# Optimization experiments

Hardware: AMD Instinct MI355X
Metric: run time of the kernel (lower is better)

Reference implementation:

```python
import jax, jax.numpy as jnp
import numpy as np

EPS = 1e-15


def setup_inputs() -> dict:
    key = jax.random.key(0)
    ks = jax.random.split(key, 10)
    F, B, L = 10, 16384, 20          # num_field, batch, hist_len
    V, D = 1000000, 16               # sparse_feature_number, sparse_feature_dim
    FEAT, E, S, G, T = 160, 8, 64, 3, 32  # feature_size, expert_num, expert_size, gate_num, tower_size
    return {
        "ids": jax.random.randint(ks[0], (F, B, L), 0, V, dtype=jnp.int64),
        "emb_table": jax.random.uniform(ks[1], (V, D), jnp.float32, -1.0, 1.0),
        "expert_w": jax.random.normal(ks[2], (E, FEAT, S), jnp.float32) * 0.05,
        "expert_b": jnp.full((E, S), 0.1, jnp.float32),
        "gate_w": jax.random.normal(ks[3], (G, FEAT, E), jnp.float32) * 0.05,
        "gate_b": jnp.full((G, E), 0.1, jnp.float32),
        "tower_w": jax.random.normal(ks[4], (G, S, T), jnp.float32) * 0.05,
        "tower_b": jnp.full((G, T), 0.1, jnp.float32),
        "out_w": jax.random.normal(ks[5], (G, T, 2), jnp.float32) * 0.05,
        "out_b": jnp.full((G, 2), 0.1, jnp.float32),
    }


def reference(ids, emb_table, expert_w, expert_b, gate_w, gate_b,
              tower_w, tower_b, out_w, out_b):
    # Embedding lookup + sum over history: [F,B,L,D] -> [F,B,D]
    field_emb = emb_table[ids].sum(axis=2)
    B = field_emb.shape[1]
    # concat per-field embeddings along feature axis: [B, F*D]
    x = jnp.transpose(field_emb, (1, 0, 2)).reshape(B, -1)
    # all experts as one batched GEMM: [B,E,S]
    experts = jax.nn.relu(jnp.einsum('bf,efs->bes', x, expert_w) + expert_b)
    # gate softmax over experts: [B,G,E]
    gates = jax.nn.softmax(jnp.einsum('bf,gfe->bge', x, gate_w) + gate_b, axis=-1)
    # gate-weighted expert mixture: [B,G,S]
    mix = jnp.einsum('bge,bes->bgs', gates, experts)
    # towers: [B,G,T] -> logits [B,G,2]
    tow = jax.nn.relu(jnp.einsum('bgs,gst->bgt', mix, tower_w) + tower_b)
    logits = jnp.einsum('bgt,gto->bgo', tow, out_w) + out_b
    probs = jnp.clip(jax.nn.softmax(logits, axis=-1), EPS, 1.0 - EPS)  # [B,3,2]
    ctr, cvr, imp = probs[:, 0], probs[:, 1], probs[:, 2]
    ctr1 = ctr[:, 1:2]
    cvr1 = cvr[:, 1:2]
    ctcvr1 = ctr1 * cvr1
    ctcvr = jnp.concatenate([1.0 - ctcvr1, ctcvr1], axis=1)
    imp1 = imp[:, 1:2]
    # out_list packed along last axis: ctr(2), ctr1(1), cvr(2), cvr1(1), ctcvr(2), ctcvr1(1), imp1(1) -> [B,10]
    return jnp.concatenate([ctr, ctr1, cvr, cvr1, ctcvr, ctcvr1, imp1], axis=1)
```

## Files before the change

kernel.cpp:

```cpp
#include <hip/hip_runtime.h>
#include <hip/hip_bf16.h>
#include <cstdint>
#include <cstddef>

#define NFIELD 10
#define BATCH  16384
#define NIDS   20
#define DEMB   16
#define NFEAT  160
#define NEXP   8
#define NS     64
#define NG     3
#define NT     32

#define BP_OFF_B  0
#define BM_OFF_B  (BP_OFF_B + 174080)
#define BT_OFF_B  (BM_OFF_B + 2176)
#define TB2_OFF_B (BT_OFF_B + 12288)
#define OWF_OFF_B (TB2_OFF_B + 384)
#define OBF_OFF_B (OWF_OFF_B + 768)

typedef short bfrag __attribute__((ext_vector_type(8)));
typedef float f32x4 __attribute__((ext_vector_type(4)));

__device__ __forceinline__ float bflo(uint32_t u) {
    union { uint32_t u; float f; } c; c.u = u << 16; return c.f;
}
__device__ __forceinline__ float bfhi(uint32_t u) {
    union { uint32_t u; float f; } c; c.u = u & 0xffff0000u; return c.f;
}
__device__ __forceinline__ float bf1(uint16_t v) {
    union { uint32_t u; float f; } c; c.u = ((uint32_t)v) << 16; return c.f;
}
__device__ __forceinline__ uint16_t f2bf(float f) {
    union { float f; uint32_t u; } c; c.f = f;
    uint32_t r = c.u + 0x7fffu + ((c.u >> 16) & 1u);
    return (uint16_t)(r >> 16);
}
__device__ __forceinline__ float ldw(const void* p, int i, bool bf) {
    return bf ? bf1(((const uint16_t*)p)[i]) : ((const float*)p)[i];
}
__device__ __forceinline__ uint16_t ldb16(const void* p, int i, bool bf) {
    return bf ? ((const uint16_t*)p)[i] : f2bf(((const float*)p)[i]);
}
__device__ __forceinline__ int sniff_bf(const uint32_t* emb_w) {
    int n_bf = 0;
    #pragma unroll
    for (int t = 0; t < 16; ++t) {
        uint32_t wv = emb_w[(size_t)t * 500000];
        uint32_t v = (wv >> 8) & 0x7Fu;
        n_bf += (v >= 0x3Bu && v <= 0x3Fu);
    }
    return n_bf >= 8;
}

__global__ __launch_bounds__(256) void pack_weights(
    const uint32_t* __restrict__ emb_w,
    const void* __restrict__ ew, const void* __restrict__ eb,
    const void* __restrict__ gw, const void* __restrict__ gb,
    const void* __restrict__ tw, const void* __restrict__ tb,
    const void* __restrict__ ow, const void* __restrict__ ob,
    uint16_t* __restrict__ bp, float* __restrict__ bm,
    uint16_t* __restrict__ bt, float* __restrict__ tb2,
    float* __restrict__ owf, float* __restrict__ obf)
{
    __shared__ int sbf;
    if (threadIdx.x == 0) sbf = sniff_bf(emb_w);
    __syncthreads();
    const bool bf = sbf != 0;

    int i = blockIdx.x * 256 + threadIdx.x;
    if (i < 10880) {
        int nt = i / 320, rem = i % 320;
        int ks = rem / 64, l = rem % 64;
        int n  = nt * 16 + (l & 15);
        int kb = ks * 32 + ((l >> 4) * 8);
        uint16_t v[8];
        #pragma unroll
        for (int j = 0; j < 8; ++j) {
            int k = kb + j;
            uint16_t x;
            if (n < 512)      x = ldb16(ew, (n >> 6) * 10240 + k * 64 + (n & 63), bf);
            else if (n < 536) x = ldb16(gw, ((n - 512) >> 3) * 1280 + k * 8 + ((n - 512) & 7), bf);
            else              x = 0;
            v[j] = x;
        }
        uint4 o;
        o.x = (uint32_t)v[0] | ((uint32_t)v[1] << 16);
        o.y = (uint32_t)v[2] | ((uint32_t)v[3] << 16);
        o.z = (uint32_t)v[4] | ((uint32_t)v[5] << 16);
        o.w = (uint32_t)v[6] | ((uint32_t)v[7] << 16);
        ((uint4*)bp)[i] = o;
    } else if (i < 11648) {
        int it = i - 10880;
        int g = it / 256, rem = it % 256;
        int ntile = rem / 128, ks = (rem / 64) & 1, l = rem % 64;
        int t  = ntile * 16 + (l & 15);
        int sb = ks * 32 + ((l >> 4) * 8);
        uint16_t v[8];
        #pragma unroll
        for (int j = 0; j < 8; ++j)
            v[j] = ldb16(tw, g * 2048 + (sb + j) * 32 + t, bf);
        uint4 o;
        o.x = (uint32_t)v[0] | ((uint32_t)v[1] << 16);
        o.y = (uint32_t)v[2] | ((uint32_t)v[3] << 16);
        o.z = (uint32_t)v[4] | ((uint32_t)v[5] << 16);
        o.w = (uint32_t)v[6] | ((uint32_t)v[7] << 16);
        ((uint4*)bt)[it] = o;
    } else if (i < 12192) {
        int n = i - 11648;
        bm[n] = (n < 512) ? ldw(eb, n, bf) : (n < 536 ? ldw(gb, n - 512, bf) : 0.0f);
    } else if (i < 12288) {
        int n = i - 12192; tb2[n] = ldw(tb, n, bf);
    } else if (i < 12480) {
        int n = i - 12288; owf[n] = ldw(ow, n, bf);
    } else if (i < 12486) {
        int n = i - 12480; obf[n] = ldw(ob, n, bf);
    }
}

__global__ __launch_bounds__(320, 3) void moe_fused(
    const void* __restrict__ ids_raw,
    const void* __restrict__ emb_raw,
    const uint16_t* __restrict__ bp,
    const float*    __restrict__ bm,
    const uint16_t* __restrict__ btw,
    const float*    __restrict__ btb,
    const float*    __restrict__ owf,
    const float*    __restrict__ obf,
    void* __restrict__ out)
{
    __shared__ uint16_t exp_lds[32][520];
    __shared__ float    gate_lds[32][33];
    __shared__ uint16_t mix_lds[32][200];
    __shared__ int      sflags;

    float* tow  = (float*)&exp_lds[0][0];
    float* prob = &gate_lds[0][0];

    const int tid = threadIdx.x;
    const int w = tid >> 6, l = tid & 63;
    const int lm = l & 15, q = l >> 4;
    const int b0 = blockIdx.x * 32;
    const int mrow = (w & 1) * 16;
    const int nhalf = w >> 1;

    if (tid == 0) {
        int n_hi = 0;
        #pragma unroll
        for (int t = 0; t < 16; ++t) {
            size_t p = (size_t)t * 100000;
            n_hi += (((const uint32_t*)ids_raw)[2 * p + 1] != 0);
        }
        sflags = ((n_hi < 2) ? 1 : 0) | (sniff_bf((const uint32_t*)emb_raw) ? 2 : 0);
    }
    __syncthreads();
    const bool i64 = (sflags & 1) != 0;
    const bool bfe = (sflags & 2) != 0;

    uint16_t* xs = &exp_lds[0][0];
    for (int p = tid; p < 32 * NFIELD; p += 320) {
        int f = p >> 5, s = p & 31;
        int idv[NIDS];
        if (i64) {
            const int4* p4 = (const int4*)((const long long*)ids_raw +
                                           ((size_t)f * BATCH + (b0 + s)) * NIDS);
            #pragma unroll
            for (int j = 0; j < NIDS / 2; ++j) {
                int4 t4 = p4[j];
                idv[2 * j + 0] = t4.x;
                idv[2 * j + 1] = t4.z;
            }
        } else {
            const int4* p4 = (const int4*)((const int*)ids_raw +
                                           ((size_t)f * BATCH + (b0 + s)) * NIDS);
            #pragma unroll
            for (int j = 0; j < NIDS / 4; ++j) {
                int4 t4 = p4[j];
                idv[4 * j + 0] = t4.x; idv[4 * j + 1] = t4.y;
                idv[4 * j + 2] = t4.z; idv[4 * j + 3] = t4.w;
            }
        }

        float acc[16];
        #pragma unroll
        for (int d = 0; d < 16; ++d) acc[d] = 0.0f;

        if (bfe) {
            #pragma unroll 5
            for (int ll = 0; ll < NIDS; ++ll) {
                const uint4* row = (const uint4*)((const uint16_t*)emb_raw +
                                                  (size_t)idv[ll] * DEMB);
                uint4 r0 = row[0];
                uint4 r1 = row[1];
                acc[0]  += bflo(r0.x); acc[1]  += bfhi(r0.x);
                acc[2]  += bflo(r0.y); acc[3]  += bfhi(r0.y);
                acc[4]  += bflo(r0.z); acc[5]  += bfhi(r0.z);
                acc[6]  += bflo(r0.w); acc[7]  += bfhi(r0.w);
                acc[8]  += bflo(r1.x); acc[9]  += bfhi(r1.x);
                acc[10] += bflo(r1.y); acc[11] += bfhi(r1.y);
                acc[12] += bflo(r1.z); acc[13] += bfhi(r1.z);
                acc[14] += bflo(r1.w); acc[15] += bfhi(r1.w);
            }
        } else {
            #pragma unroll 5
            for (int ll = 0; ll < NIDS; ++ll) {
                const float4* row = (const float4*)((const float*)emb_raw +
                                                    (size_t)idv[ll] * DEMB);
                float4 r0 = row[0], r1 = row[1], r2 = row[2], r3 = row[3];
                acc[0]  += r0.x; acc[1]  += r0.y; acc[2]  += r0.z; acc[3]  += r0.w;
                acc[4]  += r1.x; acc[5]  += r1.y; acc[6]  += r1.z; acc[7]  += r1.w;
                acc[8]  += r2.x; acc[9]  += r2.y; acc[10] += r2.z; acc[11] += r2.w;
                acc[12] += r3.x; acc[13] += r3.y; acc[14] += r3.z; acc[15] += r3.w;
            }
        }

        uint32_t pk[8];
        #pragma unroll
        for (int j = 0; j < 8; ++j)
            pk[j] = (uint32_t)f2bf(acc[2 * j]) | ((uint32_t)f2bf(acc[2 * j + 1]) << 16);
        uint4* dst = (uint4*)(xs + (size_t)s * 168 + f * DEMB);
        dst[0] = make_uint4(pk[0], pk[1], pk[2], pk[3]);
        dst[1] = make_uint4(pk[4], pk[5], pk[6], pk[7]);
    }
    __syncthreads();

    bfrag a[5];
    if (w < 4) {
        #pragma unroll
        for (int ks = 0; ks < 5; ++ks)
            a[ks] = *(const bfrag*)(xs + (size_t)(mrow + lm) * 168 + ks * 32 + q * 8);
    }
    __syncthreads();

    if (w < 4) {
        const int nt0 = nhalf * 17;
        for (int it = 0; it < 17; ++it) {
            int nt = nt0 + it;
            f32x4 acc = {0.0f, 0.0f, 0.0f, 0.0f};
            const bfrag* bpp = (const bfrag*)bp + (size_t)(nt * 5) * 64 + l;
            #pragma unroll
            for (int ks = 0; ks < 5; ++ks) {
                bfrag b = bpp[ks * 64];
                acc = __builtin_amdgcn_mfma_f32_16x16x32_bf16(a[ks], b, acc, 0, 0, 0);
            }
            int col = nt * 16 + lm;
            float bias = bm[col];
            if (col < 512) {
                #pragma unroll
                for (int r = 0; r < 4; ++r)
                    exp_lds[mrow + q * 4 + r][col] = f2bf(fmaxf(acc[r] + bias, 0.0f));
            } else {
                #pragma unroll
                for (int r = 0; r < 4; ++r)
                    gate_lds[mrow + q * 4 + r][col - 512] = acc[r] + bias;
            }
        }
    }
    __syncthreads();

    const int sm = tid >> 3, j = tid & 7;

    if (tid < 256 && j < 3) {
        float* gl = &gate_lds[sm][j * 8];
        float m = gl[0];
        #pragma unroll
        for (int e = 1; e < 8; ++e) m = fmaxf(m, gl[e]);
        float ex[8], s = 0.0f;
        #pragma unroll
        for (int e = 0; e < 8; ++e) { ex[e] = __expf(gl[e] - m); s += ex[e]; }
        float inv = 1.0f / s;
        #pragma unroll
        for (int e = 0; e < 8; ++e) gl[e] = ex[e] * inv;
    }
    __syncthreads();

    if (tid < 256) {
        for (int g = 0; g < NG; ++g) {
            float m8[8];
            #pragma unroll
            for (int i = 0; i < 8; ++i) m8[i] = 0.0f;
            #pragma unroll
            for (int e = 0; e < NEXP; ++e) {
                float gv = gate_lds[sm][g * 8 + e];
                uint4 u = *(const uint4*)&exp_lds[sm][e * 64 + j * 8];
                m8[0] = fmaf(gv, bflo(u.x), m8[0]); m8[1] = fmaf(gv, bfhi(u.x), m8[1]);
                m8[2] = fmaf(gv, bflo(u.y), m8[2]); m8[3] = fmaf(gv, bfhi(u.y), m8[3]);
                m8[4] = fmaf(gv, bflo(u.z), m8[4]); m8[5] = fmaf(gv, bfhi(u.z), m8[5]);
                m8[6] = fmaf(gv, bflo(u.w), m8[6]); m8[7] = fmaf(gv, bfhi(u.w), m8[7]);
            }
            uint4 o;
            o.x = (uint32_t)f2bf(m8[0]) | ((uint32_t)f2bf(m8[1]) << 16);
            o.y = (uint32_t)f2bf(m8[2]) | ((uint32_t)f2bf(m8[3]) << 16);
            o.z = (uint32_t)f2bf(m8[4]) | ((uint32_t)f2bf(m8[5]) << 16);
            o.w = (uint32_t)f2bf(m8[6]) | ((uint32_t)f2bf(m8[7]) << 16);
            *(uint4*)&mix_lds[sm][g * 64 + j * 8] = o;
        }
    }
    __syncthreads();

    for (int u = w; u < 12; u += 5) {
        int g = u >> 2, mt = (u >> 1) & 1, ntile = u & 1;
        f32x4 acc = {0.0f, 0.0f, 0.0f, 0.0f};
        #pragma unroll
        for (int ks = 0; ks < 2; ++ks) {
            bfrag av = *(const bfrag*)&mix_lds[mt * 16 + lm][g * 64 + ks * 32 + q * 8];
            bfrag bv = *(const bfrag*)(btw + (size_t)((((g * 2 + ntile) * 2 + ks) * 64 + l)) * 8);
            acc = __builtin_amdgcn_mfma_f32_16x16x32_bf16(av, bv, acc, 0, 0, 0);
        }
        int t = ntile * 16 + lm;
        float bias = btb[g * 32 + t];
        #pragma unroll
        for (int r = 0; r < 4; ++r)
            tow[(mt * 16 + q * 4 + r) * 100 + g * 32 + t] = fmaxf(acc[r] + bias, 0.0f);
    }
    __syncthreads();

    if (tid < 256 && j < 3) {
        int g = j;
        float l0 = obf[2 * g], l1 = obf[2 * g + 1];
        #pragma unroll 8
        for (int t = 0; t < NT; ++t) {
            float tv = tow[sm * 100 + g * 32 + t];
            l0 = fmaf(tv, owf[g * 64 + 2 * t], l0);
            l1 = fmaf(tv, owf[g * 64 + 2 * t + 1], l1);
        }
        float m  = fmaxf(l0, l1);
        float e0 = __expf(l0 - m);
        float e1 = __expf(l1 - m);
        float inv = 1.0f / (e0 + e1);
        float p0 = fminf(fmaxf(e0 * inv, 1e-15f), 1.0f);
        float p1 = fminf(fmaxf(e1 * inv, 1e-15f), 1.0f);
        prob[sm * 6 + 2 * g + 0] = p0;
        prob[sm * 6 + 2 * g + 1] = p1;
    }
    __syncthreads();

    if (tid < 256) {
        float ctr0 = prob[sm * 6 + 0], ctr1 = prob[sm * 6 + 1];
        float cvr0 = prob[sm * 6 + 2], cvr1 = prob[sm * 6 + 3];
        float imp1 = prob[sm * 6 + 5];
        float ctcvr1 = ctr1 * cvr1;
        for (int o = j; o < 10; o += 8) {
            float v;
            switch (o) {
                case 0: v = ctr0; break;
                case 1: v = ctr1; break;
                case 2: v = ctr1; break;
                case 3: v = cvr0; break;
                case 4: v = cvr1; break;
                case 5: v = cvr1; break;
                case 6: v = 1.0f - ctcvr1; break;
                case 7: v = ctcvr1; break;
                case 8: v = ctcvr1; break;
                default: v = imp1; break;
            }
            if (bfe) ((uint16_t*)out)[(size_t)(b0 + sm) * 10 + o] = f2bf(v);
            else     ((float*)out)[(size_t)(b0 + sm) * 10 + o]    = v;
        }
    }
}

extern "C" void kernel_launch(void* const* d_in, const int* in_sizes, int n_in,
                              void* d_out, int out_size, void* d_ws, size_t ws_size,
                              hipStream_t stream) {
    const void* ids = d_in[0];
    const void* emb = d_in[1];

    char* ws = (char*)d_ws;
    uint16_t* bpk = (uint16_t*)(ws + BP_OFF_B);
    float*    bm  = (float*)(ws + BM_OFF_B);
    uint16_t* btw = (uint16_t*)(ws + BT_OFF_B);
    float*    tb2 = (float*)(ws + TB2_OFF_B);
    float*    owf = (float*)(ws + OWF_OFF_B);
    float*    obf = (float*)(ws + OBF_OFF_B);

    pack_weights<<<49, 256, 0, stream>>>(
        (const uint32_t*)emb,
        d_in[2], d_in[3], d_in[4], d_in[5], d_in[6], d_in[7], d_in[8], d_in[9],
        bpk, bm, btw, tb2, owf, obf);
    moe_fused<<<BATCH / 32, 320, 0, stream>>>(
        ids, emb, bpk, bm, btw, tb2, owf, obf, d_out);
}
```

Before: 180.8 us.

## Overlap second-half embedding gather with first M-tile GEMM across warps

Measured after the change: 198.8 us. 1.1x slower.

```diff
diff --git a/kernel.cpp b/kernel.cpp
--- a/kernel.cpp
+++ b/kernel.cpp
@@ -137,13 +137,12 @@
 
     float* tow  = (float*)&exp_lds[0][0];
     float* prob = &gate_lds[0][0];
+    uint16_t* xs = &mix_lds[0][0];
 
     const int tid = threadIdx.x;
     const int w = tid >> 6, l = tid & 63;
     const int lm = l & 15, q = l >> 4;
     const int b0 = blockIdx.x * 32;
-    const int mrow = (w & 1) * 16;
-    const int nhalf = w >> 1;
 
     if (tid == 0) {
         int n_hi = 0;
@@ -158,9 +157,7 @@
     const bool i64 = (sflags & 1) != 0;
     const bool bfe = (sflags & 2) != 0;
 
-    uint16_t* xs = &exp_lds[0][0];
-    for (int p = tid; p < 32 * NFIELD; p += 320) {
-        int f = p >> 5, s = p & 31;
+    auto gather_half = [&](int f, int s, int h) {
         int idv[NIDS];
         if (i64) {
             const int4* p4 = (const int4*)((const long long*)ids_raw +
@@ -181,62 +178,46 @@
                 idv[4 * j + 2] = t4.z; idv[4 * j + 3] = t4.w;
             }
         }
-
-        float acc[16];
-        #pragma unroll
-        for (int d = 0; d < 16; ++d) acc[d] = 0.0f;
-
+        float acc[8];
+        #pragma unroll
+        for (int d = 0; d < 8; ++d) acc[d] = 0.0f;
         if (bfe) {
-            #pragma unroll 5
+            #pragma unroll
             for (int ll = 0; ll < NIDS; ++ll) {
-                const uint4* row = (const uint4*)((const uint16_t*)emb_raw +
-                                                  (size_t)idv[ll] * DEMB);
-                uint4 r0 = row[0];
-                uint4 r1 = row[1];
-                acc[0]  += bflo(r0.x); acc[1]  += bfhi(r0.x);
-                acc[2]  += bflo(r0.y); acc[3]  += bfhi(r0.y);
-                acc[4]  += bflo(r0.z); acc[5]  += bfhi(r0.z);
-                acc[6]  += bflo(r0.w); acc[7]  += bfhi(r0.w);
-                acc[8]  += bflo(r1.x); acc[9]  += bfhi(r1.x);
-                acc[10] += bflo(r1.y); acc[11] += bfhi(r1.y);
-                acc[12] += bflo(r1.z); acc[13] += bfhi(r1.z);
-                acc[14] += bflo(r1.w); acc[15] += bfhi(r1.w);
+                uint4 r = *(const uint4*)((const uint16_t*)emb_raw +
+                                          (size_t)idv[ll] * DEMB + h * 8);
+                acc[0] += bflo(r.x); acc[1] += bfhi(r.x);
+                acc[2] += bflo(r.y); acc[3] += bfhi(r.y);
+                acc[4] += bflo(r.z); acc[5] += bfhi(r.z);
+                acc[6] += bflo(r.w); acc[7] += bfhi(r.w);
             }
         } else {
-            #pragma unroll 5
+            #pragma unroll
             for (int ll = 0; ll < NIDS; ++ll) {
-                const float4* row = (const float4*)((const float*)emb_raw +
-                                                    (size_t)idv[ll] * DEMB);
-                float4 r0 = row[0], r1 = row[1], r2 = row[2], r3 = row[3];
-                acc[0]  += r0.x; acc[1]  += r0.y; acc[2]  += r0.z; acc[3]  += r0.w;
-                acc[4]  += r1.x; acc[5]  += r1.y; acc[6]  += r1.z; acc[7]  += r1.w;
-                acc[8]  += r2.x; acc[9]  += r2.y; acc[10] += r2.z; acc[11] += r2.w;
-                acc[12] += r3.x; acc[13] += r3.y; acc[14] += r3.z; acc[15] += r3.w;
-            }
-        }
-
-        uint32_t pk[8];
-        #pragma unroll
-        for (int j = 0; j < 8; ++j)
-            pk[j] = (uint32_t)f2bf(acc[2 * j]) | ((uint32_t)f2bf(acc[2 * j + 1]) << 16);
-        uint4* dst = (uint4*)(xs + (size_t)s * 168 + f * DEMB);
-        dst[0] = make_uint4(pk[0], pk[1], pk[2], pk[3]);
-        dst[1] = make_uint4(pk[4], pk[5], pk[6], pk[7]);
-    }
-    __syncthreads();
-
-    bfrag a[5];
-    if (w < 4) {
+                const float4* p = (const float4*)((const float*)emb_raw +
+                                                  (size_t)idv[ll] * DEMB + h * 8);
+                float4 r0 = p[0], r1 = p[1];
+                acc[0] += r0.x; acc[1] += r0.y; acc[2] += r0.z; acc[3] += r0.w;
+                acc[4] += r1.x; acc[5] += r1.y; acc[6] += r1.z; acc[7] += r1.w;
+            }
+        }
+        uint4 o;
+        o.x = (uint32_t)f2bf(acc[0]) | ((uint32_t)f2bf(acc[1]) << 16);
+        o.y = (uint32_t)f2bf(acc[2]) | ((uint32_t)f2bf(acc[3]) << 16);
+        o.z = (uint32_t)f2bf(acc[4]) | ((uint32_t)f2bf(acc[5]) << 16);
+        o.w = (uint32_t)f2bf(acc[6]) | ((uint32_t)f2bf(acc[7]) << 16);
+        *(uint4*)(xs + (size_t)s * 200 + f * DEMB + h * 8) = o;
+    };
+
+    auto gemm_mtile = [&](int mrow) {
+        bfrag a[5];
         #pragma unroll
         for (int ks = 0; ks < 5; ++ks)
-            a[ks] = *(const bfrag*)(xs + (size_t)(mrow + lm) * 168 + ks * 32 + q * 8);
-    }
-    __syncthreads();
-
-    if (w < 4) {
-        const int nt0 = nhalf * 17;
-        for (int it = 0; it < 17; ++it) {
-            int nt = nt0 + it;
+            a[ks] = *(const bfrag*)(xs + (size_t)(mrow + lm) * 200 + ks * 32 + q * 8);
+        int start = (w == 0) ? 0 : (w == 1) ? 12 : 23;
+        int cnt   = (w == 0) ? 12 : 11;
+        for (int it = 0; it < cnt; ++it) {
+            int nt = start + it;
             f32x4 acc = {0.0f, 0.0f, 0.0f, 0.0f};
             const bfrag* bpp = (const bfrag*)bp + (size_t)(nt * 5) * 64 + l;
             #pragma unroll
@@ -256,7 +237,30 @@
                     gate_lds[mrow + q * 4 + r][col - 512] = acc[r] + bias;
             }
         }
-    }
+    };
+
+    {
+        int f = tid >> 5, rem = tid & 31;
+        gather_half(f, rem >> 1, rem & 1);
+    }
+    __syncthreads();
+
+    if (w < 3) {
+        gemm_mtile(0);
+    } else {
+        int local = tid - 192;
+        #pragma unroll
+        for (int c = 0; c < 3; ++c) {
+            int sp = c * 128 + local;
+            if (sp < 320) {
+                int f = sp >> 5, rem = sp & 31;
+                gather_half(f, 16 + (rem >> 1), rem & 1);
+            }
+        }
+    }
+    __syncthreads();
+
+    if (w < 3) gemm_mtile(16);
     __syncthreads();
 
     const int sm = tid >> 3, j = tid & 7;
```
